# Performance work log

Hardware: AMD Instinct MI355X
Metric: run time of the kernel (lower is better)

Reference implementation:

```python
import jax, jax.numpy as jnp
import numpy as np

A = 2048        # atoms
IN_DEPTH = 128
OUT_DEPTH = 128
FILTER_LEN = 16


def setup_inputs() -> dict:
    key = jax.random.key(0)
    k1, k2, k3, k4 = jax.random.split(key, 4)
    node_property_tensor = jax.random.normal(k1, (A, IN_DEPTH), dtype=jnp.float32)
    connectivity_tensor = jax.random.normal(k2, (A, A, FILTER_LEN), dtype=jnp.float32)
    bond_property_tensor = jax.random.normal(k3, (A, FILTER_LEN, 2), dtype=jnp.float32)
    # filters initialized ~ N(0,1) * 1/in_depth, per the torch init
    filters = jax.random.normal(k4, (OUT_DEPTH, FILTER_LEN, IN_DEPTH + 2), dtype=jnp.float32) / IN_DEPTH
    return {
        "node_property_tensor": node_property_tensor,
        "connectivity_tensor": connectivity_tensor,
        "bond_property_tensor": bond_property_tensor,
        "filters": filters,
    }


def reference(node_property_tensor, connectivity_tensor, bond_property_tensor, filters):
    # gather neighbor features: conn (A,B,F) x node (B,D) -> (A,F,D)
    node_connection = jnp.einsum('abf,bd->afd', connectivity_tensor, node_property_tensor)
    # append bond properties -> (A, F, D+2)
    combined = jnp.concatenate([node_connection, bond_property_tensor], axis=2)
    # fused broadcast-multiply + double-sum: (A,F,K) x (O,F,K) -> (A,O)
    return jnp.einsum('afk,ofk->ao', combined, filters)
```

## Files before the change

kernel.cpp:

```cpp
#include <hip/hip_runtime.h>
#include <stdint.h>

#define N_ATOM 2048
#define K_TOT  32768
#define KCH    2048
#define BK2    128
#define NIT    (KCH / BK2)

typedef __attribute__((ext_vector_type(8))) short bf16x8;
typedef __attribute__((ext_vector_type(4))) float f32x4;

typedef __attribute__((address_space(3))) uint32_t lds_u32;
typedef __attribute__((address_space(1))) uint32_t gbl_u32;

__device__ __forceinline__ void async_ld16(const void* g, void* l) {
  __builtin_amdgcn_global_load_lds((const gbl_u32*)g, (lds_u32*)l, 16, 0, 0);
}

__device__ __forceinline__ unsigned short f2bf(float x) {
  union { float f; uint32_t u; } v; v.f = x;
  uint32_t r = v.u + 0x7FFFu + ((v.u >> 16) & 1u);
  return (unsigned short)(r >> 16);
}

__device__ __forceinline__ uint32_t pack_bf2(float x, float y) {
  union { float f; uint32_t u; } a, b;
  a.f = x; b.f = y;
  uint32_t au = a.u + 0x7FFFu;
  uint32_t bu = b.u + 0x7FFFu;
  return __builtin_amdgcn_perm(bu, au, 0x07060302u);
}

__global__ __launch_bounds__(256) void k_gt(const float* __restrict__ node,
                                            const float* __restrict__ filt,
                                            unsigned short* __restrict__ Gt) {
  __shared__ unsigned short As[128 * 136];
  __shared__ unsigned short Bs[128 * 136];
  const int t  = threadIdx.x;
  const int b0 = blockIdx.x * 128;
  const int n0 = blockIdx.y * 128;

#pragma unroll
  for (int rep = 0; rep < 16; ++rep) {
    int q = rep * 256 + t;
    int row = q >> 5, c4 = q & 31;
    float4 v = *(const float4*)(node + (size_t)(b0 + row) * 128 + c4 * 4);
    unsigned short* dst = &As[row * 136 + c4 * 4];
    dst[0] = f2bf(v.x); dst[1] = f2bf(v.y); dst[2] = f2bf(v.z); dst[3] = f2bf(v.w);
  }
#pragma unroll
  for (int rep = 0; rep < 32; ++rep) {
    int q = rep * 256 + t;
    int row = q >> 6, c2 = q & 63;
    float2 v = *(const float2*)(filt + (size_t)(n0 + row) * 130 + c2 * 2);
    unsigned short* dst = &Bs[row * 136 + c2 * 2];
    dst[0] = f2bf(v.x); dst[1] = f2bf(v.y);
  }
  __syncthreads();

  const int w = t >> 6, l = t & 63;
  const int lm = l & 15, q4 = l >> 4;

  f32x4 acc[2][8];
#pragma unroll
  for (int ms = 0; ms < 2; ++ms)
#pragma unroll
    for (int ns = 0; ns < 8; ++ns)
      acc[ms][ns] = (f32x4){0.f, 0.f, 0.f, 0.f};

#pragma unroll
  for (int ks = 0; ks < 4; ++ks) {
    int ko = ks * 32 + q4 * 8;
    bf16x8 a[2], b[8];
#pragma unroll
    for (int ms = 0; ms < 2; ++ms) {
      int m = w * 32 + ms * 16 + lm;
      a[ms] = *(const bf16x8*)&As[m * 136 + ko];
    }
#pragma unroll
    for (int ns = 0; ns < 8; ++ns) {
      int n = ns * 16 + lm;
      b[ns] = *(const bf16x8*)&Bs[n * 136 + ko];
    }
#pragma unroll
    for (int ms = 0; ms < 2; ++ms)
#pragma unroll
      for (int ns = 0; ns < 8; ++ns)
        acc[ms][ns] = __builtin_amdgcn_mfma_f32_16x16x32_bf16(a[ms], b[ns], acc[ms][ns], 0, 0, 0);
  }

#pragma unroll
  for (int ms = 0; ms < 2; ++ms)
#pragma unroll
    for (int ns = 0; ns < 8; ++ns)
#pragma unroll
      for (int i = 0; i < 4; ++i) {
        int m = w * 32 + ms * 16 + q4 * 4 + i;
        int n = ns * 16 + lm;
        Gt[(size_t)(b0 + m) * 2048 + n0 + n] = f2bf(acc[ms][ns][i]);
      }
}

__global__ __launch_bounds__(256) void k_bond(const float* __restrict__ bond,
                                              const float* __restrict__ filt,
                                              float* __restrict__ out) {
  __shared__ float fb[128 * 32];
  __shared__ float bl[16 * 32];
  const int t  = threadIdx.x;
  const int a0 = blockIdx.x * 16;

#pragma unroll
  for (int r = 0; r < 16; ++r) {
    int idx = r * 256 + t;
    int o = idx >> 5, fj = idx & 31;
    int f = fj >> 1, j = fj & 1;
    fb[idx] = filt[(size_t)o * 2080 + f * 130 + 128 + j];
  }
  bl[t]       = bond[(size_t)a0 * 32 + t];
  bl[256 + t] = bond[(size_t)a0 * 32 + 256 + t];
  __syncthreads();

#pragma unroll
  for (int r = 0; r < 8; ++r) {
    int idx = r * 256 + t;
    int aa = idx >> 7, o = idx & 127;
    const float2* bp = (const float2*)&bl[aa * 32];
    const float2* fp = (const float2*)&fb[o * 32];
    float acc = 0.f;
#pragma unroll
    for (int f = 0; f < 16; ++f) {
      float2 b2 = bp[f], f2 = fp[f];
      acc += b2.x * f2.x + b2.y * f2.y;
    }
    out[(size_t)(a0 + aa) * 128 + o] = acc;
  }
}

__global__ __launch_bounds__(512, 2) void k_main(const float* __restrict__ conn,
                                                 const unsigned short* __restrict__ Gt,
                                                 float* __restrict__ out) {
  __shared__ unsigned short Bh[2][8 * 128 * 16];

  const int t  = threadIdx.x;
  const int w  = t >> 6, l = t & 63;
  const int lm = l & 15, q4 = l >> 4;
  const int a0 = blockIdx.x * 128;
  const int kc = blockIdx.y * KCH;

  f32x4 acc[8];
#pragma unroll
  for (int ns = 0; ns < 8; ++ns)
    acc[ns] = (f32x4){0.f, 0.f, 0.f, 0.f};

  const float* arow = conn + (size_t)(a0 + w * 16 + lm) * K_TOT;

  auto stageB = [&](int buf, int k0) {
    const char* gB = (const char*)(Gt + (size_t)k0 * 128);
#pragma unroll
    for (int r = 0; r < 4; ++r) {
      const void* g = gB + (size_t)(r * 512 + t) * 16;
      void* lb = (void*)((char*)&Bh[buf][0] + r * 8192 + w * 1024);
      async_ld16(g, lb);
    }
  };

  f32x4 Ar[4][2];
  auto loadA = [&](int k0) {
#pragma unroll
    for (int kk = 0; kk < 4; ++kk) {
      const float* p = arow + k0 + kk * 32 + q4 * 8;
      Ar[kk][0] = __builtin_nontemporal_load((const f32x4*)p);
      Ar[kk][1] = __builtin_nontemporal_load((const f32x4*)(p + 4));
    }
  };

  stageB(0, kc);
  loadA(kc);
  __syncthreads();

  for (int it = 0; it < NIT; ++it) {
    const int cur = it & 1;

    bf16x8 af[4];
#pragma unroll
    for (int kk = 0; kk < 4; ++kk) {
      f32x4 lo = Ar[kk][0], hi = Ar[kk][1];
      union { bf16x8 v; uint32_t u[4]; } cvt;
      cvt.u[0] = pack_bf2(lo[0], lo[1]);
      cvt.u[1] = pack_bf2(lo[2], lo[3]);
      cvt.u[2] = pack_bf2(hi[0], hi[1]);
      cvt.u[3] = pack_bf2(hi[2], hi[3]);
      af[kk] = cvt.v;
    }

    if (it + 1 < NIT) {
      stageB(1 - cur, kc + (it + 1) * BK2);
      loadA(kc + (it + 1) * BK2);
    }

#pragma unroll
    for (int kk = 0; kk < 4; ++kk) {
      const int b_rel = 2 * kk + (q4 >> 1);
      const int f0 = (q4 & 1) * 8;
#pragma unroll
      for (int ns = 0; ns < 8; ++ns) {
        int o = ns * 16 + lm;
        bf16x8 b = *(const bf16x8*)&Bh[cur][b_rel * 2048 + o * 16 + f0];
        acc[ns] = __builtin_amdgcn_mfma_f32_16x16x32_bf16(af[kk], b, acc[ns], 0, 0, 0);
      }
    }

    __syncthreads();
  }

#pragma unroll
  for (int ns = 0; ns < 8; ++ns)
#pragma unroll
    for (int i = 0; i < 4; ++i) {
      int m = w * 16 + q4 * 4 + i;
      int n = ns * 16 + lm;
      atomicAdd(&out[(size_t)(a0 + m) * 128 + n], acc[ns][i]);
    }
}

extern "C" void kernel_launch(void* const* d_in, const int* in_sizes, int n_in,
                              void* d_out, int out_size, void* d_ws, size_t ws_size,
                              hipStream_t stream) {
  const float* node = (const float*)d_in[0];
  const float* conn = (const float*)d_in[1];
  const float* bond = (const float*)d_in[2];
  const float* filt = (const float*)d_in[3];
  float* out = (float*)d_out;

  if (ws_size < (size_t)N_ATOM * 2048 * sizeof(unsigned short)) return;
  unsigned short* Gt = (unsigned short*)d_ws;

  k_gt  <<<dim3(16, 16), 256, 0, stream>>>(node, filt, Gt);
  k_bond<<<dim3(128),    256, 0, stream>>>(bond, filt, out);
  k_main<<<dim3(16, 16), 512, 0, stream>>>(conn, Gt, out);
}
```

Measured before the change: 419.1 us.

## Merge precompute kernels and deepen A-register prefetch with manual waitcnt barriers

Fuses the Gt-precompute and bond-term kernels into one launch that dispatches on block index, removing one kernel launch. In the main GEMM, the fp32 connectivity tile is now double-buffered in registers two iterations ahead. __syncthreads is replaced with explicit vmcnt waits plus s_barrier so outstanding A loads can stay in flight across the barrier. This raises register pressure at 512 threads with 2 blocks per CU, and hand-counted vmcnt values are fragile if the compiler reorders the loads.

After: 413.3 us. No clear change (-1.4%).

```diff
diff --git a/kernel.cpp b/kernel.cpp
--- a/kernel.cpp
+++ b/kernel.cpp
@@ -31,108 +31,110 @@
   return __builtin_amdgcn_perm(bu, au, 0x07060302u);
 }
 
-__global__ __launch_bounds__(256) void k_gt(const float* __restrict__ node,
-                                            const float* __restrict__ filt,
-                                            unsigned short* __restrict__ Gt) {
-  __shared__ unsigned short As[128 * 136];
-  __shared__ unsigned short Bs[128 * 136];
-  const int t  = threadIdx.x;
-  const int b0 = blockIdx.x * 128;
-  const int n0 = blockIdx.y * 128;
-
-#pragma unroll
-  for (int rep = 0; rep < 16; ++rep) {
-    int q = rep * 256 + t;
-    int row = q >> 5, c4 = q & 31;
-    float4 v = *(const float4*)(node + (size_t)(b0 + row) * 128 + c4 * 4);
-    unsigned short* dst = &As[row * 136 + c4 * 4];
-    dst[0] = f2bf(v.x); dst[1] = f2bf(v.y); dst[2] = f2bf(v.z); dst[3] = f2bf(v.w);
-  }
-#pragma unroll
-  for (int rep = 0; rep < 32; ++rep) {
-    int q = rep * 256 + t;
-    int row = q >> 6, c2 = q & 63;
-    float2 v = *(const float2*)(filt + (size_t)(n0 + row) * 130 + c2 * 2);
-    unsigned short* dst = &Bs[row * 136 + c2 * 2];
-    dst[0] = f2bf(v.x); dst[1] = f2bf(v.y);
-  }
-  __syncthreads();
-
-  const int w = t >> 6, l = t & 63;
-  const int lm = l & 15, q4 = l >> 4;
-
-  f32x4 acc[2][8];
-#pragma unroll
-  for (int ms = 0; ms < 2; ++ms)
-#pragma unroll
-    for (int ns = 0; ns < 8; ++ns)
-      acc[ms][ns] = (f32x4){0.f, 0.f, 0.f, 0.f};
-
-#pragma unroll
-  for (int ks = 0; ks < 4; ++ks) {
-    int ko = ks * 32 + q4 * 8;
-    bf16x8 a[2], b[8];
-#pragma unroll
-    for (int ms = 0; ms < 2; ++ms) {
-      int m = w * 32 + ms * 16 + lm;
-      a[ms] = *(const bf16x8*)&As[m * 136 + ko];
-    }
-#pragma unroll
-    for (int ns = 0; ns < 8; ++ns) {
-      int n = ns * 16 + lm;
-      b[ns] = *(const bf16x8*)&Bs[n * 136 + ko];
-    }
+__global__ __launch_bounds__(256) void k_pre(const float* __restrict__ node,
+                                             const float* __restrict__ filt,
+                                             const float* __restrict__ bond,
+                                             unsigned short* __restrict__ Gt,
+                                             float* __restrict__ out) {
+  __shared__ unsigned short SM[2 * 128 * 136];
+  const int t   = threadIdx.x;
+  const int bid = blockIdx.x;
+
+  if (bid < 256) {
+    unsigned short* As = SM;
+    unsigned short* Bs = SM + 128 * 136;
+    const int b0 = (bid & 15) * 128;
+    const int n0 = (bid >> 4) * 128;
+
+#pragma unroll
+    for (int rep = 0; rep < 16; ++rep) {
+      int q = rep * 256 + t;
+      int row = q >> 5, c4 = q & 31;
+      float4 v = *(const float4*)(node + (size_t)(b0 + row) * 128 + c4 * 4);
+      unsigned short* dst = &As[row * 136 + c4 * 4];
+      dst[0] = f2bf(v.x); dst[1] = f2bf(v.y); dst[2] = f2bf(v.z); dst[3] = f2bf(v.w);
+    }
+#pragma unroll
+    for (int rep = 0; rep < 32; ++rep) {
+      int q = rep * 256 + t;
+      int row = q >> 6, c2 = q & 63;
+      float2 v = *(const float2*)(filt + (size_t)(n0 + row) * 130 + c2 * 2);
+      unsigned short* dst = &Bs[row * 136 + c2 * 2];
+      dst[0] = f2bf(v.x); dst[1] = f2bf(v.y);
+    }
+    __syncthreads();
+
+    const int w = t >> 6, l = t & 63;
+    const int lm = l & 15, q4 = l >> 4;
+
+    f32x4 acc[2][8];
 #pragma unroll
     for (int ms = 0; ms < 2; ++ms)
 #pragma unroll
       for (int ns = 0; ns < 8; ++ns)
-        acc[ms][ns] = __builtin_amdgcn_mfma_f32_16x16x32_bf16(a[ms], b[ns], acc[ms][ns], 0, 0, 0);
-  }
-
-#pragma unroll
-  for (int ms = 0; ms < 2; ++ms)
-#pragma unroll
-    for (int ns = 0; ns < 8; ++ns)
-#pragma unroll
-      for (int i = 0; i < 4; ++i) {
-        int m = w * 32 + ms * 16 + q4 * 4 + i;
+        acc[ms][ns] = (f32x4){0.f, 0.f, 0.f, 0.f};
+
+#pragma unroll
+    for (int ks = 0; ks < 4; ++ks) {
+      int ko = ks * 32 + q4 * 8;
+      bf16x8 a[2], b[8];
+#pragma unroll
+      for (int ms = 0; ms < 2; ++ms) {
+        int m = w * 32 + ms * 16 + lm;
+        a[ms] = *(const bf16x8*)&As[m * 136 + ko];
+      }
+#pragma unroll
+      for (int ns = 0; ns < 8; ++ns) {
         int n = ns * 16 + lm;
-        Gt[(size_t)(b0 + m) * 2048 + n0 + n] = f2bf(acc[ms][ns][i]);
-      }
-}
-
-__global__ __launch_bounds__(256) void k_bond(const float* __restrict__ bond,
-                                              const float* __restrict__ filt,
-                                              float* __restrict__ out) {
-  __shared__ float fb[128 * 32];
-  __shared__ float bl[16 * 32];
-  const int t  = threadIdx.x;
-  const int a0 = blockIdx.x * 16;
-
-#pragma unroll
-  for (int r = 0; r < 16; ++r) {
-    int idx = r * 256 + t;
-    int o = idx >> 5, fj = idx & 31;
-    int f = fj >> 1, j = fj & 1;
-    fb[idx] = filt[(size_t)o * 2080 + f * 130 + 128 + j];
-  }
-  bl[t]       = bond[(size_t)a0 * 32 + t];
-  bl[256 + t] = bond[(size_t)a0 * 32 + 256 + t];
-  __syncthreads();
-
-#pragma unroll
-  for (int r = 0; r < 8; ++r) {
-    int idx = r * 256 + t;
-    int aa = idx >> 7, o = idx & 127;
-    const float2* bp = (const float2*)&bl[aa * 32];
-    const float2* fp = (const float2*)&fb[o * 32];
-    float acc = 0.f;
-#pragma unroll
-    for (int f = 0; f < 16; ++f) {
-      float2 b2 = bp[f], f2 = fp[f];
-      acc += b2.x * f2.x + b2.y * f2.y;
-    }
-    out[(size_t)(a0 + aa) * 128 + o] = acc;
+        b[ns] = *(const bf16x8*)&Bs[n * 136 + ko];
+      }
+#pragma unroll
+      for (int ms = 0; ms < 2; ++ms)
+#pragma unroll
+        for (int ns = 0; ns < 8; ++ns)
+          acc[ms][ns] = __builtin_amdgcn_mfma_f32_16x16x32_bf16(a[ms], b[ns], acc[ms][ns], 0, 0, 0);
+    }
+
+#pragma unroll
+    for (int ms = 0; ms < 2; ++ms)
+#pragma unroll
+      for (int ns = 0; ns < 8; ++ns)
+#pragma unroll
+        for (int i = 0; i < 4; ++i) {
+          int m = w * 32 + ms * 16 + q4 * 4 + i;
+          int n = ns * 16 + lm;
+          Gt[(size_t)(b0 + m) * 2048 + n0 + n] = f2bf(acc[ms][ns][i]);
+        }
+  } else {
+    float* fb = (float*)SM;
+    float* bl = (float*)SM + 128 * 32;
+    const int a0 = (bid - 256) * 16;
+
+#pragma unroll
+    for (int r = 0; r < 16; ++r) {
+      int idx = r * 256 + t;
+      int o = idx >> 5, fj = idx & 31;
+      int f = fj >> 1, j = fj & 1;
+      fb[idx] = filt[(size_t)o * 2080 + f * 130 + 128 + j];
+    }
+    bl[t]       = bond[(size_t)a0 * 32 + t];
+    bl[256 + t] = bond[(size_t)a0 * 32 + 256 + t];
+    __syncthreads();
+
+#pragma unroll
+    for (int r = 0; r < 8; ++r) {
+      int idx = r * 256 + t;
+      int aa = idx >> 7, o = idx & 127;
+      const float2* bp = (const float2*)&bl[aa * 32];
+      const float2* fp = (const float2*)&fb[o * 32];
+      float acc = 0.f;
+#pragma unroll
+      for (int f = 0; f < 16; ++f) {
+        float2 b2 = bp[f], f2 = fp[f];
+        acc += b2.x * f2.x + b2.y * f2.y;
+      }
+      out[(size_t)(a0 + aa) * 128 + o] = acc;
+    }
   }
 }
 
@@ -164,27 +166,34 @@
     }
   };
 
-  f32x4 Ar[4][2];
-  auto loadA = [&](int k0) {
-#pragma unroll
-    for (int kk = 0; kk < 4; ++kk) {
-      const float* p = arow + k0 + kk * 32 + q4 * 8;
-      Ar[kk][0] = __builtin_nontemporal_load((const f32x4*)p);
-      Ar[kk][1] = __builtin_nontemporal_load((const f32x4*)(p + 4));
-    }
-  };
+  f32x4 Ar[2][4][2];
+#define LOADA(BUF, K0)                                                      \
+  do {                                                                      \
+    _Pragma("unroll") for (int kk = 0; kk < 4; ++kk) {                      \
+      const float* p = arow + (K0) + kk * 32 + q4 * 8;                      \
+      Ar[BUF][kk][0] = __builtin_nontemporal_load((const f32x4*)p);         \
+      Ar[BUF][kk][1] = __builtin_nontemporal_load((const f32x4*)(p + 4));   \
+    }                                                                       \
+  } while (0)
 
   stageB(0, kc);
-  loadA(kc);
-  __syncthreads();
-
+  LOADA(0, kc);
+  LOADA(1, kc + BK2);
+  __builtin_amdgcn_sched_barrier(0);
+  asm volatile("s_waitcnt vmcnt(16)" ::: "memory");
+  __builtin_amdgcn_s_barrier();
+  __builtin_amdgcn_sched_barrier(0);
+
+#pragma unroll
   for (int it = 0; it < NIT; ++it) {
     const int cur = it & 1;
 
+    if (it + 1 < NIT) stageB(1 - cur, kc + (it + 1) * BK2);
+
     bf16x8 af[4];
 #pragma unroll
     for (int kk = 0; kk < 4; ++kk) {
-      f32x4 lo = Ar[kk][0], hi = Ar[kk][1];
+      f32x4 lo = Ar[cur][kk][0], hi = Ar[cur][kk][1];
       union { bf16x8 v; uint32_t u[4]; } cvt;
       cvt.u[0] = pack_bf2(lo[0], lo[1]);
       cvt.u[1] = pack_bf2(lo[2], lo[3]);
@@ -193,10 +202,7 @@
       af[kk] = cvt.v;
     }
 
-    if (it + 1 < NIT) {
-      stageB(1 - cur, kc + (it + 1) * BK2);
-      loadA(kc + (it + 1) * BK2);
-    }
+    if (it + 2 < NIT) LOADA(cur, kc + (it + 2) * BK2);
 
 #pragma unroll
     for (int kk = 0; kk < 4; ++kk) {
@@ -210,8 +216,18 @@
       }
     }
 
-    __syncthreads();
+    if (it + 1 < NIT) {
+      __builtin_amdgcn_sched_barrier(0);
+      if (it + 2 < NIT) {
+        asm volatile("s_waitcnt vmcnt(8)" ::: "memory");
+      } else {
+        asm volatile("s_waitcnt vmcnt(0)" ::: "memory");
+      }
+      __builtin_amdgcn_s_barrier();
+      __builtin_amdgcn_sched_barrier(0);
+    }
   }
+#undef LOADA
 
 #pragma unroll
   for (int ns = 0; ns < 8; ++ns)
@@ -235,7 +251,6 @@
   if (ws_size < (size_t)N_ATOM * 2048 * sizeof(unsigned short)) return;
   unsigned short* Gt = (unsigned short*)d_ws;
 
-  k_gt  <<<dim3(16, 16), 256, 0, stream>>>(node, filt, Gt);
-  k_bond<<<dim3(128),    256, 0, stream>>>(bond, filt, out);
+  k_pre <<<dim3(384),    256, 0, stream>>>(node, filt, bond, Gt, out);
   k_main<<<dim3(16, 16), 512, 0, stream>>>(conn, Gt, out);
 }
```
